# Kernel optimization log

Hardware: AMD Instinct MI355X
Metric: run time of the kernel (lower is better)

The kernel has to match this reference:

```python
import jax, jax.numpy as jnp
import numpy as np

OVERFLOW_MARGIN = 1e-08


def setup_inputs() -> dict:
    key = jax.random.key(0)
    k1, k2, k3 = jax.random.split(key, 3)
    N, D, OUT = 8192, 256, 128
    values = jax.random.normal(k1, (N, D), dtype=jnp.float32)
    # adjacency: positive dense weights, self-connected (add identity)
    adjacency = jax.random.uniform(k2, (N, N), dtype=jnp.float32) + jnp.eye(N, dtype=jnp.float32)
    W = jax.random.normal(k3, (D, OUT), dtype=jnp.float32) * (1.0 / np.sqrt(D))
    b = jnp.zeros((OUT,), dtype=jnp.float32)
    return {"values": values, "adjacency": adjacency, "W": W, "b": b}


def reference(values, adjacency, W, b):
    # fc_sc = Dense(values)
    fc = values @ W + b                                   # [N, OUT]
    # symmetric degree normalization: L = D^{-1/2} A D^{-1/2}
    d = jnp.sum(adjacency, axis=1, keepdims=True)         # [N, 1] == A @ ones
    d_inv_sqrt = (d + OVERFLOW_MARGIN) ** -0.5            # [N, 1]
    # L @ fc expressed as elementwise row/col scaling around one GEMM
    # (mathematically identical to diag(dinv) @ A @ diag(dinv) @ fc)
    out = d_inv_sqrt * (adjacency @ (d_inv_sqrt * fc))    # [N, OUT]
    return out
```

## Files before the change

kernel.cpp:

```cpp
#include <hip/hip_runtime.h>
#include <hip/hip_bf16.h>
#include <stdint.h>

#define N_NODES 8192
#define D_IN 256
#define D_OUT 128
#define BKK 64
#define KSPLIT 2

typedef __bf16 bf16x8 __attribute__((ext_vector_type(8)));
typedef __bf16 bf16x4 __attribute__((ext_vector_type(4)));
typedef float f32x4 __attribute__((ext_vector_type(4)));

__global__ __launch_bounds__(256) void k_prep(const float* __restrict__ A,
                                              __bf16* __restrict__ Abf,
                                              float* __restrict__ dinv) {
  const int r = blockIdx.x;
  const int t = threadIdx.x;
  const f32x4* row = (const f32x4*)(A + (size_t)r * N_NODES);
  bf16x4* orow = (bf16x4*)(Abf + (size_t)r * N_NODES);
  float s = 0.f;
#pragma unroll
  for (int i = 0; i < 8; ++i) {
    f32x4 v = __builtin_nontemporal_load(&row[t + i * 256]);
    s += (v[0] + v[1]) + (v[2] + v[3]);
    bf16x4 h;
    h[0] = (__bf16)v[0]; h[1] = (__bf16)v[1]; h[2] = (__bf16)v[2]; h[3] = (__bf16)v[3];
    orow[t + i * 256] = h;
  }
#pragma unroll
  for (int off = 32; off > 0; off >>= 1) s += __shfl_down(s, off, 64);
  __shared__ float wsum[4];
  if ((t & 63) == 0) wsum[t >> 6] = s;
  __syncthreads();
  if (t == 0) {
    float d = ((wsum[0] + wsum[1]) + (wsum[2] + wsum[3])) + 1e-8f;
    dinv[r] = 1.0f / sqrtf(d);
  }
}

#define VPAD 260
__global__ __launch_bounds__(256) void k_fc(const float* __restrict__ values,
                                            const float* __restrict__ W,
                                            const float* __restrict__ bias,
                                            const float* __restrict__ dinv,
                                            __bf16* __restrict__ yT) {
  __shared__ float vsm[32 * VPAD];
  const int t = threadIdx.x;
  const int rb = blockIdx.x * 32;
  {
    const float4* src = (const float4*)(values + (size_t)rb * D_IN);
#pragma unroll
    for (int i = 0; i < 8; ++i) {
      int f = t + i * 256;
      int r = f >> 6, kq = f & 63;
      *(float4*)(vsm + r * VPAD + kq * 4) = src[f];
    }
  }
  __syncthreads();
  const int tr = t >> 5, tc = t & 31;
  const int c0 = tc * 4;
  float accm[4][4] = {};
  const float* vr = vsm + (tr * 4) * VPAD;
#pragma unroll 4
  for (int k4 = 0; k4 < 64; ++k4) {
    f32x4 a[4];
    float4 wv[4];
#pragma unroll
    for (int i = 0; i < 4; ++i) a[i] = *(const f32x4*)(vr + i * VPAD + k4 * 4);
#pragma unroll
    for (int kk = 0; kk < 4; ++kk) wv[kk] = *(const float4*)(W + (size_t)(k4 * 4 + kk) * D_OUT + c0);
#pragma unroll
    for (int i = 0; i < 4; ++i) {
      accm[i][0] += a[i][0] * wv[0].x + a[i][1] * wv[1].x + a[i][2] * wv[2].x + a[i][3] * wv[3].x;
      accm[i][1] += a[i][0] * wv[0].y + a[i][1] * wv[1].y + a[i][2] * wv[2].y + a[i][3] * wv[3].y;
      accm[i][2] += a[i][0] * wv[0].z + a[i][1] * wv[1].z + a[i][2] * wv[2].z + a[i][3] * wv[3].z;
      accm[i][3] += a[i][0] * wv[0].w + a[i][1] * wv[1].w + a[i][2] * wv[2].w + a[i][3] * wv[3].w;
    }
  }
  const int rg = rb + tr * 4;
  float dv[4];
#pragma unroll
  for (int i = 0; i < 4; ++i) dv[i] = dinv[rg + i];
#pragma unroll
  for (int j = 0; j < 4; ++j) {
    const int c = c0 + j;
    const float bc = bias[c];
    bf16x4 p;
#pragma unroll
    for (int i = 0; i < 4; ++i) p[i] = (__bf16)((accm[i][j] + bc) * dv[i]);
    *(bf16x4*)(yT + (size_t)c * N_NODES + rg) = p;
  }
}

__device__ __forceinline__ void gload_lds16(const void* gp, void* lp) {
  __builtin_amdgcn_global_load_lds((const __attribute__((address_space(1))) void*)gp,
                                   (__attribute__((address_space(3))) void*)lp, 16, 0, 0);
}

__global__ __launch_bounds__(256) void k_gemm(const __bf16* __restrict__ Abf,
                                              const __bf16* __restrict__ yT,
                                              float* __restrict__ partial) {
  __shared__ __align__(16) char smA[2][32 * 128];
  __shared__ __align__(16) char smB[2][128 * 128];
  const int t = threadIdx.x;
  const int l = t & 63;
  const int w = t >> 6;
  const int mb = blockIdx.x * 32;
  const int k0 = blockIdx.y * (N_NODES / KSPLIT);
  float* pout = partial + (size_t)blockIdx.y * N_NODES * D_OUT;

  const int am = t >> 3, aseg = t & 7;
  const __bf16* agp = Abf + (size_t)(mb + am) * N_NODES + k0 + ((aseg ^ (am & 7)) * 8);
  const int bn_base = w * 8 + (l >> 3);
  const int bseg = l & 7;

  f32x4 acc00 = {}, acc01 = {}, acc10 = {}, acc11 = {};
  const int lr = l & 15;
  const int lg = l >> 4;

  int aoff[2][2], boff[2][2];
#pragma unroll
  for (int mf = 0; mf < 2; ++mf)
#pragma unroll
    for (int ks = 0; ks < 2; ++ks) {
      int m = mf * 16 + lr;
      int seg = ks * 4 + lg;
      aoff[mf][ks] = m * 128 + ((seg ^ (m & 7)) * 16);
      int n = w * 32 + mf * 16 + lr;
      boff[mf][ks] = n * 128 + ((seg ^ (n & 7)) * 16);
    }

  auto stage = [&](int kb, int buf) {
    gload_lds16(agp + kb, (void*)(&smA[buf][0] + w * 1024));
#pragma unroll
    for (int q = 0; q < 4; ++q) {
      int n = q * 32 + bn_base;
      const __bf16* gp = yT + (size_t)n * N_NODES + k0 + kb + ((bseg ^ (n & 7)) * 8);
      gload_lds16(gp, (void*)(&smB[buf][0] + q * 4096 + w * 1024));
    }
  };

  stage(0, 0);
  __syncthreads();

  const int KSTEPS = (N_NODES / KSPLIT) / BKK;
  int cur = 0;
  for (int step = 0; step < KSTEPS; ++step) {
    const int nxt = cur ^ 1;
    if (step + 1 < KSTEPS) stage((step + 1) * BKK, nxt);
#pragma unroll
    for (int ks = 0; ks < 2; ++ks) {
      bf16x8 af0 = *(const bf16x8*)(&smA[cur][0] + aoff[0][ks]);
      bf16x8 af1 = *(const bf16x8*)(&smA[cur][0] + aoff[1][ks]);
      bf16x8 bq0 = *(const bf16x8*)(&smB[cur][0] + boff[0][ks]);
      bf16x8 bq1 = *(const bf16x8*)(&smB[cur][0] + boff[1][ks]);
      acc00 = __builtin_amdgcn_mfma_f32_16x16x32_bf16(af0, bq0, acc00, 0, 0, 0);
      acc01 = __builtin_amdgcn_mfma_f32_16x16x32_bf16(af0, bq1, acc01, 0, 0, 0);
      acc10 = __builtin_amdgcn_mfma_f32_16x16x32_bf16(af1, bq0, acc10, 0, 0, 0);
      acc11 = __builtin_amdgcn_mfma_f32_16x16x32_bf16(af1, bq1, acc11, 0, 0, 0);
    }
    __syncthreads();
    cur = nxt;
  }

#pragma unroll
  for (int mf = 0; mf < 2; ++mf) {
#pragma unroll
    for (int nf = 0; nf < 2; ++nf) {
      f32x4 a = (mf == 0) ? ((nf == 0) ? acc00 : acc01) : ((nf == 0) ? acc10 : acc11);
      const int col = w * 32 + nf * 16 + lr;
      const int rowb = mb + mf * 16 + lg * 4;
#pragma unroll
      for (int v2 = 0; v2 < 4; ++v2) {
        pout[(size_t)(rowb + v2) * D_OUT + col] = a[v2];
      }
    }
  }
}

__global__ __launch_bounds__(256) void k_finish(const float* __restrict__ partial,
                                                const float* __restrict__ dinv,
                                                float* __restrict__ out) {
  const int i = blockIdx.x * 256 + threadIdx.x;
  const f32x4* p0 = (const f32x4*)partial;
  const f32x4* p1 = (const f32x4*)(partial + (size_t)N_NODES * D_OUT);
  f32x4 a = p0[i] + p1[i];
  const float dv = dinv[i >> 5];
  f32x4* o = (f32x4*)out;
  o[i] = a * dv;
}

extern "C" void kernel_launch(void* const* d_in, const int* in_sizes, int n_in,
                              void* d_out, int out_size, void* d_ws, size_t ws_size,
                              hipStream_t stream) {
  const float* values = (const float*)d_in[0];
  const float* A = (const float*)d_in[1];
  const float* W = (const float*)d_in[2];
  const float* bias = (const float*)d_in[3];
  float* out = (float*)d_out;

  char* ws = (char*)d_ws;
  float* dinv = (float*)ws;
  __bf16* yT = (__bf16*)(ws + (64 << 10));
  float* partial = (float*)(ws + (4 << 20));
  __bf16* Abf = (__bf16*)(ws + (16 << 20));

  k_prep<<<N_NODES, 256, 0, stream>>>(A, Abf, dinv);
  k_fc<<<N_NODES / 32, 256, 0, stream>>>(values, W, bias, dinv, yT);
  k_gemm<<<dim3(N_NODES / 32, KSPLIT), 256, 0, stream>>>(Abf, yT, partial);
  k_finish<<<N_NODES * D_OUT / 4 / 256, 256, 0, stream>>>(partial, dinv, out);
}
```

Measured before the change: 456.2 us.

## Deepen k_gemm LDS pipeline to four stages with explicit vmcnt waits

Replaces the double-buffered LDS staging in the aggregation GEMM with a four-deep ring of buffers. Three tiles are kept in flight, guarded by explicit s_waitcnt vmcnt counts and raw s_barrier calls. Fragments are read into registers before the buffer is refilled, so the refill can overlap the MFMAs. This is meant to hide global-load latency in a kernel that is memory-bound on the bf16 adjacency stream. The trade-off is twice the LDS per block, which may lower occupancy, and correctness now depends on the hand-counted vmcnt of 15 (5 loads per stage times 3 stages).

```diff
diff --git a/kernel.cpp b/kernel.cpp
--- a/kernel.cpp
+++ b/kernel.cpp
@@ -7,6 +7,7 @@
 #define D_OUT 128
 #define BKK 64
 #define KSPLIT 2
+#define KSTEPS (N_NODES / KSPLIT / BKK)
 
 typedef __bf16 bf16x8 __attribute__((ext_vector_type(8)));
 typedef __bf16 bf16x4 __attribute__((ext_vector_type(4)));
@@ -101,8 +102,8 @@
 __global__ __launch_bounds__(256) void k_gemm(const __bf16* __restrict__ Abf,
                                               const __bf16* __restrict__ yT,
                                               float* __restrict__ partial) {
-  __shared__ __align__(16) char smA[2][32 * 128];
-  __shared__ __align__(16) char smB[2][128 * 128];
+  __shared__ __align__(16) char smA[4][32 * 128];
+  __shared__ __align__(16) char smB[4][128 * 128];
   const int t = threadIdx.x;
   const int l = t & 63;
   const int w = t >> 6;
@@ -141,27 +142,42 @@
     }
   };
 
-  stage(0, 0);
-  __syncthreads();
-
-  const int KSTEPS = (N_NODES / KSPLIT) / BKK;
-  int cur = 0;
-  for (int step = 0; step < KSTEPS; ++step) {
-    const int nxt = cur ^ 1;
-    if (step + 1 < KSTEPS) stage((step + 1) * BKK, nxt);
-#pragma unroll
-    for (int ks = 0; ks < 2; ++ks) {
-      bf16x8 af0 = *(const bf16x8*)(&smA[cur][0] + aoff[0][ks]);
-      bf16x8 af1 = *(const bf16x8*)(&smA[cur][0] + aoff[1][ks]);
-      bf16x8 bq0 = *(const bf16x8*)(&smB[cur][0] + boff[0][ks]);
-      bf16x8 bq1 = *(const bf16x8*)(&smB[cur][0] + boff[1][ks]);
-      acc00 = __builtin_amdgcn_mfma_f32_16x16x32_bf16(af0, bq0, acc00, 0, 0, 0);
-      acc01 = __builtin_amdgcn_mfma_f32_16x16x32_bf16(af0, bq1, acc01, 0, 0, 0);
-      acc10 = __builtin_amdgcn_mfma_f32_16x16x32_bf16(af1, bq0, acc10, 0, 0, 0);
-      acc11 = __builtin_amdgcn_mfma_f32_16x16x32_bf16(af1, bq1, acc11, 0, 0, 0);
-    }
-    __syncthreads();
-    cur = nxt;
+  stage(0 * BKK, 0);
+  stage(1 * BKK, 1);
+  stage(2 * BKK, 2);
+  stage(3 * BKK, 3);
+
+  for (int t_i = 0; t_i < KSTEPS; ++t_i) {
+    const int b = t_i & 3;
+    if (t_i < KSTEPS - 4) {
+      asm volatile("s_waitcnt vmcnt(15)" ::: "memory");
+    } else {
+      asm volatile("s_waitcnt vmcnt(0)" ::: "memory");
+    }
+    __builtin_amdgcn_s_barrier();
+
+    bf16x8 af0a = *(const bf16x8*)(&smA[b][0] + aoff[0][0]);
+    bf16x8 af1a = *(const bf16x8*)(&smA[b][0] + aoff[1][0]);
+    bf16x8 bq0a = *(const bf16x8*)(&smB[b][0] + boff[0][0]);
+    bf16x8 bq1a = *(const bf16x8*)(&smB[b][0] + boff[1][0]);
+    bf16x8 af0b = *(const bf16x8*)(&smA[b][0] + aoff[0][1]);
+    bf16x8 af1b = *(const bf16x8*)(&smA[b][0] + aoff[1][1]);
+    bf16x8 bq0b = *(const bf16x8*)(&smB[b][0] + boff[0][1]);
+    bf16x8 bq1b = *(const bf16x8*)(&smB[b][0] + boff[1][1]);
+    asm volatile("s_waitcnt lgkmcnt(0)" ::: "memory");
+    __builtin_amdgcn_sched_barrier(0);
+    __builtin_amdgcn_s_barrier();
+
+    if (t_i + 4 < KSTEPS) stage((t_i + 4) * BKK, b);
+
+    acc00 = __builtin_amdgcn_mfma_f32_16x16x32_bf16(af0a, bq0a, acc00, 0, 0, 0);
+    acc01 = __builtin_amdgcn_mfma_f32_16x16x32_bf16(af0a, bq1a, acc01, 0, 0, 0);
+    acc10 = __builtin_amdgcn_mfma_f32_16x16x32_bf16(af1a, bq0a, acc10, 0, 0, 0);
+    acc11 = __builtin_amdgcn_mfma_f32_16x16x32_bf16(af1a, bq1a, acc11, 0, 0, 0);
+    acc00 = __builtin_amdgcn_mfma_f32_16x16x32_bf16(af0b, bq0b, acc00, 0, 0, 0);
+    acc01 = __builtin_amdgcn_mfma_f32_16x16x32_bf16(af0b, bq1b, acc01, 0, 0, 0);
+    acc10 = __builtin_amdgcn_mfma_f32_16x16x32_bf16(af1b, bq0b, acc10, 0, 0, 0);
+    acc11 = __builtin_amdgcn_mfma_f32_16x16x32_bf16(af1b, bq1b, acc11, 0, 0, 0);
   }
 
 #pragma unroll
```

Measured after the change: 444.4 us. 1.03x faster.
